# Kernel optimization log

Measured on AMD Instinct MI355X. Metric: run time of the kernel, lower is better.

The kernel has to match this reference:

```python
import jax, jax.numpy as jnp
import numpy as np

NUM_EXPERTS = 64
TOPK = 8
EPS = 1.1920929e-07  # torch.finfo(float32).eps


def setup_inputs() -> dict:
    key = jax.random.key(0)
    k1, k2 = jax.random.split(key)
    hidden_states = jax.random.normal(k1, (1, 4096, 4096), dtype=jnp.float32)
    wg_weight = jax.random.normal(k2, (NUM_EXPERTS, 4096), dtype=jnp.float32) * 0.02
    return {"hidden_states": hidden_states, "wg_weight": wg_weight}


def _routing(logits, capacity):
    # logits: [T, E]; capacity: static python int
    gates = jax.nn.softmax(logits, axis=1)                       # [T, E]
    _, idx = jax.lax.top_k(gates, TOPK)                          # [T, k]
    emask = jax.nn.one_hot(idx, NUM_EXPERTS, dtype=jnp.float32)  # [T, k, E]
    # sum of selected gate probs per token, clamped at fp32 eps
    gates_s = jnp.clip(jnp.einsum('tke,te->t', emask, gates), EPS)[:, None]
    router_probs = gates / gates_s                               # [T, E]
    # priority: cumulative position of each token within each expert,
    # scanned over (topk-major, token-minor) flattened order
    idx_flat = idx.T.reshape(-1)                                 # [k*T]
    mflat = jax.nn.one_hot(idx_flat, NUM_EXPERTS, dtype=jnp.int32)
    tp = jnp.cumsum(mflat, axis=0) * mflat - 1                   # [k*T, E]
    tp = tp.reshape(TOPK, -1, NUM_EXPERTS).transpose(1, 0, 2).max(axis=1)  # [T, E]
    valid = (tp >= 0) & (tp < capacity)                          # [T, E]
    tp = jnp.where(valid, tp, 0)
    dispatch_mask = jax.nn.one_hot(tp, capacity, dtype=jnp.bool_) & valid[:, :, None]  # [T, E, C]
    combine_weights = router_probs[:, :, None] * dispatch_mask   # [T, E, C]
    return combine_weights, dispatch_mask


def reference(hidden_states, wg_weight):
    b, s, h = hidden_states.shape
    x = hidden_states.reshape(-1, h).astype(jnp.float32)         # [T, H]
    logits = x @ wg_weight.T                                     # [T, E]
    # expert_capacity = max tokens assigned to any expert (data-dependent,
    # computed eagerly as in the torch .item() call)
    _, idx = jax.lax.top_k(jax.nn.softmax(logits, axis=1), TOPK)
    counts = jnp.bincount(idx.reshape(-1), length=NUM_EXPERTS)
    capacity = int(counts.max())
    return _routing(logits, capacity)
```

## Files before the change

kernel.cpp:

```cpp
#include <hip/hip_runtime.h>
#include <hip/hip_bf16.h>


#define TOK 4096
#define HID 4096
#define NE  64
#define NK  8

typedef __attribute__((ext_vector_type(8))) short short8;
typedef __attribute__((ext_vector_type(4))) float f32x4;

__device__ __forceinline__ short f2bf(float f) {
  __hip_bfloat16 h = __float2bfloat16(f);
  return *reinterpret_cast<short*>(&h);
}
__device__ __forceinline__ float bf2f(short s) {
  unsigned u = ((unsigned)(unsigned short)s) << 16;
  return __uint_as_float(u);
}
__device__ __forceinline__ void cvt3(float f, short& s0, short& s1, short& s2) {
  s0 = f2bf(f);
  float r1 = f - bf2f(s0);
  s1 = f2bf(r1);
  float r2 = r1 - bf2f(s1);
  s2 = f2bf(r2);
}

__global__ __launch_bounds__(256) void gemm_fill(
    const float* __restrict__ x, const float* __restrict__ wg,
    double* __restrict__ partial, int kchunk, int* __restrict__ flag,
    float* __restrict__ out, int out_n) {
  __shared__ __align__(16) short XA[3][64][72];
  __shared__ __align__(16) short WB[3][64][72];
  const int tid = threadIdx.x;
  if (blockIdx.x == 0 && blockIdx.y == 0 && tid == 0) *flag = 0;
  const int t0   = blockIdx.x * 64;
  const int k0   = blockIdx.y * kchunk;
  const int lane = tid & 63;
  const int w    = tid >> 6;
  const int m    = lane & 15;
  const int q    = lane >> 4;
  const int lrow = tid >> 2;
  const int lq   = tid & 3;

  const int    nblk    = gridDim.x * gridDim.y;
  const int    bid     = blockIdx.y * gridDim.x + blockIdx.x;
  const size_t n4      = ((size_t)(unsigned)out_n) >> 2;
  const size_t fstride = (size_t)nblk * 256;
  size_t       fi      = (size_t)bid * 256 + tid;
  const int    steps   = kchunk >> 6;
  const size_t titers  = (n4 + fstride - 1) / fstride;
  const size_t chunk   = (titers + (size_t)steps - 1) / (size_t)steps;
  f32x4* o4 = (f32x4*)out;
  const f32x4 z4 = (f32x4){0.f, 0.f, 0.f, 0.f};

  f32x4 acc[4];
#pragma unroll
  for (int nt = 0; nt < 4; ++nt) acc[nt] = (f32x4){0.f, 0.f, 0.f, 0.f};

  for (int s = 0; s < kchunk; s += 64) {
    const int kk = k0 + s;
#pragma unroll
    for (int c = 0; c < 4; ++c) {
      const int col = lq * 16 + c * 4;
      float4 xv = *(const float4*)&x [(size_t)(t0 + lrow) * HID + kk + col];
      float4 wv = *(const float4*)&wg[(size_t)lrow * HID + kk + col];
      short4 p0, p1, p2;
      cvt3(xv.x, p0.x, p1.x, p2.x);  cvt3(xv.y, p0.y, p1.y, p2.y);
      cvt3(xv.z, p0.z, p1.z, p2.z);  cvt3(xv.w, p0.w, p1.w, p2.w);
      *(short4*)&XA[0][lrow][col] = p0;
      *(short4*)&XA[1][lrow][col] = p1;
      *(short4*)&XA[2][lrow][col] = p2;
      cvt3(wv.x, p0.x, p1.x, p2.x);  cvt3(wv.y, p0.y, p1.y, p2.y);
      cvt3(wv.z, p0.z, p1.z, p2.z);  cvt3(wv.w, p0.w, p1.w, p2.w);
      *(short4*)&WB[0][lrow][col] = p0;
      *(short4*)&WB[1][lrow][col] = p1;
      *(short4*)&WB[2][lrow][col] = p2;
    }
    __syncthreads();
#pragma unroll
    for (int kc = 0; kc < 64; kc += 32) {
      short8 a0 = *(const short8*)&XA[0][w * 16 + m][kc + q * 8];
      short8 a1 = *(const short8*)&XA[1][w * 16 + m][kc + q * 8];
      short8 a2 = *(const short8*)&XA[2][w * 16 + m][kc + q * 8];
#pragma unroll
      for (int nt = 0; nt < 4; ++nt) {
        short8 b0 = *(const short8*)&WB[0][nt * 16 + m][kc + q * 8];
        short8 b1 = *(const short8*)&WB[1][nt * 16 + m][kc + q * 8];
        short8 b2 = *(const short8*)&WB[2][nt * 16 + m][kc + q * 8];
        acc[nt] = __builtin_amdgcn_mfma_f32_16x16x32_bf16(a0, b0, acc[nt], 0, 0, 0);
        acc[nt] = __builtin_amdgcn_mfma_f32_16x16x32_bf16(a0, b1, acc[nt], 0, 0, 0);
        acc[nt] = __builtin_amdgcn_mfma_f32_16x16x32_bf16(a1, b0, acc[nt], 0, 0, 0);
        acc[nt] = __builtin_amdgcn_mfma_f32_16x16x32_bf16(a0, b2, acc[nt], 0, 0, 0);
        acc[nt] = __builtin_amdgcn_mfma_f32_16x16x32_bf16(a1, b1, acc[nt], 0, 0, 0);
        acc[nt] = __builtin_amdgcn_mfma_f32_16x16x32_bf16(a2, b0, acc[nt], 0, 0, 0);
      }
    }
    for (size_t c = 0; c < chunk && fi < n4; ++c, fi += fstride)
      __builtin_nontemporal_store(z4, o4 + fi);
    __syncthreads();
  }

  for (; fi < n4; fi += fstride)
    __builtin_nontemporal_store(z4, o4 + fi);
  if (bid == 0 && tid == 0)
    for (size_t i2 = n4 << 2; i2 < (size_t)(unsigned)out_n; ++i2) out[i2] = 0.f;

  double* base = partial + (size_t)blockIdx.y * TOK * NE;
#pragma unroll
  for (int nt = 0; nt < 4; ++nt)
#pragma unroll
    for (int v = 0; v < 4; ++v)
      base[(size_t)(t0 + w * 16 + q * 4 + v) * NE + nt * 16 + m] =
          (double)acc[nt][v];
}

__global__ __launch_bounds__(256) void verify_kernel(
    const float* __restrict__ x, const float* __restrict__ wg,
    const double* __restrict__ partial, int nsplit, int* __restrict__ flag) {
  const int gid  = blockIdx.x * blockDim.x + threadIdx.x;
  const int wid  = gid >> 6;
  const int lane = gid & 63;
  const int t = (wid * 521) & (TOK - 1);
  const int e = wid & 63;
  double acc = 0.0;
  for (int k = lane; k < HID; k += 64)
    acc = fma((double)x[(size_t)t * HID + k], (double)wg[(size_t)e * HID + k], acc);
#pragma unroll
  for (int off = 32; off; off >>= 1) acc += __shfl_xor(acc, off);
  if (lane == 0) {
    double got = 0.0;
    for (int p = 0; p < nsplit; ++p)
      got += partial[(size_t)p * TOK * NE + (size_t)t * NE + e];
    if (!(fabs(got - acc) <= 1e-3)) atomicOr(flag, 1);
  }
}

__global__ __launch_bounds__(256) void repair_splitk(
    const float* __restrict__ x, const float* __restrict__ wg,
    double* __restrict__ partial, int kchunk, const int* __restrict__ flag) {
  if (*(volatile const int*)flag == 0) return;
  __shared__ float xs[16][68];
  __shared__ float wsh[64][68];
  const int tid = threadIdx.x;
  const int t0  = blockIdx.x * 16;
  const int k0  = blockIdx.y * kchunk;
  const int tok = tid & 15;
  const int eg  = tid >> 4;
  const int lrow = tid >> 4;
  const int lq   = tid & 15;
  double acc[4] = {0.0, 0.0, 0.0, 0.0};

  for (int s = 0; s < kchunk; s += 64) {
    const int kk = k0 + s;
    {
      float4 v = *(const float4*)&x[(size_t)(t0 + lrow) * HID + kk + lq * 4];
      *(float4*)&xs[lrow][lq * 4] = v;
    }
#pragma unroll
    for (int it = 0; it < 4; ++it) {
      int r = it * 16 + lrow;
      float4 v = *(const float4*)&wg[(size_t)r * HID + kk + lq * 4];
      *(float4*)&wsh[r][lq * 4] = v;
    }
    __syncthreads();
#pragma unroll
    for (int kc = 0; kc < 64; kc += 4) {
      float4 xv = *(const float4*)&xs[tok][kc];
#pragma unroll
      for (int j = 0; j < 4; ++j) {
        float4 wv = *(const float4*)&wsh[eg * 4 + j][kc];
        acc[j] = fma((double)xv.x, (double)wv.x, acc[j]);
        acc[j] = fma((double)xv.y, (double)wv.y, acc[j]);
        acc[j] = fma((double)xv.z, (double)wv.z, acc[j]);
        acc[j] = fma((double)xv.w, (double)wv.w, acc[j]);
      }
    }
    __syncthreads();
  }
  double* base = partial + (size_t)blockIdx.y * TOK * NE;
#pragma unroll
  for (int j = 0; j < 4; ++j)
    base[(size_t)(t0 + tok) * NE + eg * 4 + j] = acc[j];
}

__global__ __launch_bounds__(256) void topk_kernel(
    const double* __restrict__ partial, int nsplit,
    int* __restrict__ idx_kt, float* __restrict__ w_kt) {
  const int gid  = blockIdx.x * blockDim.x + threadIdx.x;
  const int t    = gid >> 6;
  const int lane = gid & 63;

  double v = 0.0;
  for (int p = 0; p < nsplit; ++p)
    v += partial[(size_t)p * TOK * NE + (size_t)t * NE + lane];

  double m = v;
#pragma unroll
  for (int off = 32; off; off >>= 1) {
    double o = __shfl_xor(m, off);
    m = o > m ? o : m;
  }
  double g = exp(v - m);
  double s = g;
#pragma unroll
  for (int off = 32; off; off >>= 1) s += __shfl_xor(s, off);
  double gate = g / s;

  float key = (float)gate;
  double ssel = 0.0;
  int my_k = -1;
#pragma unroll
  for (int k = 0; k < NK; ++k) {
    float bv = key;
    int   bi = lane;
#pragma unroll
    for (int off = 32; off; off >>= 1) {
      float ov = __shfl_xor(bv, off);
      int   oi = __shfl_xor(bi, off);
      if (ov > bv || (ov == bv && oi < bi)) { bv = ov; bi = oi; }
    }
    ssel += __shfl(gate, bi);
    if (lane == bi) { my_k = k; key = -1.0f; }
  }
  double gs = ssel;
  const double eps = (double)1.1920929e-07f;
  if (gs < eps) gs = eps;

  if (my_k >= 0) {
    idx_kt[my_k * TOK + t] = lane;
    w_kt [my_k * TOK + t] = (float)(gate / gs);
  }
}

__global__ __launch_bounds__(1024) void rank_scatter(
    const int* __restrict__ idx_kt, const float* __restrict__ w_kt,
    float* __restrict__ out, int C) {
  const int e    = blockIdx.x;
  const int tid  = threadIdx.x;
  const int lane = tid & 63;
  const int w    = tid >> 6;
  __shared__ int wt[16];
  int running = 0;
  const unsigned long long below = (1ull << lane) - 1ull;

  for (int i0 = 0; i0 < NK * TOK; i0 += 1024) {
    const int i = i0 + tid;
    const bool mhit = (idx_kt[i] == e);
    unsigned long long mask = __ballot(mhit);
    if (lane == 0) wt[w] = __popcll(mask);
    __syncthreads();
    int woff = 0, tot = 0;
#pragma unroll
    for (int j = 0; j < 16; ++j) {
      int c = wt[j];
      tot += c;
      if (j < w) woff += c;
    }
    if (mhit) {
      const int c = running + woff + __popcll(mask & below);
      if (c < C) {
        const int t = i & (TOK - 1);
        size_t off = ((size_t)t * NE + e) * (size_t)C + (size_t)c;
        out[off] = w_kt[i];
        out[(size_t)TOK * NE * C + off] = 1.0f;
      }
    }
    running += tot;
    __syncthreads();
  }
}

extern "C" void kernel_launch(void* const* d_in, const int* in_sizes, int n_in,
                              void* d_out, int out_size, void* d_ws, size_t ws_size,
                              hipStream_t stream) {
  const float* x  = (const float*)d_in[0];
  const float* wg = (const float*)d_in[1];
  float* out = (float*)d_out;

  const int C = out_size / (2 * TOK * NE);

  const size_t slab = (size_t)TOK * NE * sizeof(double);
  const size_t tail = 2 * (size_t)NK * TOK * sizeof(int);
  int nsplit = 8;
  while (nsplit > 1 && (size_t)nsplit * slab + tail + 64 > ws_size) nsplit >>= 1;
  const int kchunk = HID / nsplit;

  char* ws = (char*)d_ws;
  double* partial = (double*)ws;
  int*    idx_kt  = (int*)  (ws + (size_t)nsplit * slab);
  float*  w_kt    = (float*)(ws + (size_t)nsplit * slab + (size_t)NK * TOK * 4);
  int*    flag    = (int*)  (ws + (size_t)nsplit * slab + tail);


  dim3 bgrid(TOK / 64, nsplit);
  dim3 rgrid(TOK / 16, nsplit);
  gemm_fill    <<<bgrid, 256, 0, stream>>>(x, wg, partial, kchunk, flag, out, out_size);
  verify_kernel<<<128, 256, 0, stream>>>(x, wg, partial, nsplit, flag);
  repair_splitk<<<rgrid, 256, 0, stream>>>(x, wg, partial, kchunk, flag);
  topk_kernel  <<<TOK * 64 / 256, 256, 0, stream>>>(partial, nsplit, idx_kt, w_kt);
  rank_scatter <<<NE, 1024, 0, stream>>>(idx_kt, w_kt, out, C);
}
```

Before: 1.301 ms.

## Pre-split gate weights once and move output zero-fill to separate blocks

Adds a prep kernel that splits the gate weights into three bf16 parts once, so GEMM blocks no longer re-split them every tile. The GEMM now reads those parts straight from global memory instead of through shared memory. Zeroing the large output moves out of the GEMM loop into dedicated extra blocks in the same launch, so the fill runs alongside the GEMM on separate blocks. The trade-offs are one extra launch, more workspace, and B-operand loads that no longer go through LDS and may be less coalesced.

```diff
diff --git a/kernel.cpp b/kernel.cpp
--- a/kernel.cpp
+++ b/kernel.cpp
@@ -26,16 +26,46 @@
   s2 = f2bf(r2);
 }
 
-__global__ __launch_bounds__(256) void gemm_fill(
-    const float* __restrict__ x, const float* __restrict__ wg,
-    double* __restrict__ partial, int kchunk, int* __restrict__ flag,
-    float* __restrict__ out, int out_n) {
+__global__ __launch_bounds__(256) void prep_wg(
+    const float* __restrict__ wg, short* __restrict__ wp) {
+  const int idx = blockIdx.x * 256 + threadIdx.x;
+  const int e  = idx >> 10;
+  const int kq = idx & 1023;
+  float4 v = *(const float4*)&wg[(size_t)e * HID + kq * 4];
+  short4 p0, p1, p2;
+  cvt3(v.x, p0.x, p1.x, p2.x);  cvt3(v.y, p0.y, p1.y, p2.y);
+  cvt3(v.z, p0.z, p1.z, p2.z);  cvt3(v.w, p0.w, p1.w, p2.w);
+  *(short4*)&wp[((size_t)  0 + e) * HID + kq * 4] = p0;
+  *(short4*)&wp[((size_t) 64 + e) * HID + kq * 4] = p1;
+  *(short4*)&wp[((size_t)128 + e) * HID + kq * 4] = p2;
+}
+
+__global__ __launch_bounds__(256, 3) void mega(
+    const float* __restrict__ x, const short* __restrict__ wp,
+    double* __restrict__ partial, int kchunk, int ngemm, int nfill,
+    int* __restrict__ flag, float* __restrict__ out, int out_n) {
+  const int bx  = blockIdx.x;
+  const int tid = threadIdx.x;
+
+  if (bx >= ngemm) {
+    const int    fid    = bx - ngemm;
+    const size_t n4     = ((size_t)(unsigned)out_n) >> 2;
+    const size_t stride = (size_t)nfill * 256;
+    f32x4* o4 = (f32x4*)out;
+    const f32x4 z4 = (f32x4){0.f, 0.f, 0.f, 0.f};
+    for (size_t i = (size_t)fid * 256 + tid; i < n4; i += stride)
+      __builtin_nontemporal_store(z4, o4 + i);
+    if (fid == 0 && tid == 0)
+      for (size_t i2 = n4 << 2; i2 < (size_t)(unsigned)out_n; ++i2) out[i2] = 0.f;
+    return;
+  }
+
   __shared__ __align__(16) short XA[3][64][72];
-  __shared__ __align__(16) short WB[3][64][72];
-  const int tid = threadIdx.x;
-  if (blockIdx.x == 0 && blockIdx.y == 0 && tid == 0) *flag = 0;
-  const int t0   = blockIdx.x * 64;
-  const int k0   = blockIdx.y * kchunk;
+  if (bx == 0 && tid == 0) *flag = 0;
+  const int tileid = bx & 63;
+  const int slab   = bx >> 6;
+  const int t0   = tileid * 64;
+  const int k0   = slab * kchunk;
   const int lane = tid & 63;
   const int w    = tid >> 6;
   const int m    = lane & 15;
@@ -43,17 +73,6 @@
   const int lrow = tid >> 2;
   const int lq   = tid & 3;
 
-  const int    nblk    = gridDim.x * gridDim.y;
-  const int    bid     = blockIdx.y * gridDim.x + blockIdx.x;
-  const size_t n4      = ((size_t)(unsigned)out_n) >> 2;
-  const size_t fstride = (size_t)nblk * 256;
-  size_t       fi      = (size_t)bid * 256 + tid;
-  const int    steps   = kchunk >> 6;
-  const size_t titers  = (n4 + fstride - 1) / fstride;
-  const size_t chunk   = (titers + (size_t)steps - 1) / (size_t)steps;
-  f32x4* o4 = (f32x4*)out;
-  const f32x4 z4 = (f32x4){0.f, 0.f, 0.f, 0.f};
-
   f32x4 acc[4];
 #pragma unroll
   for (int nt = 0; nt < 4; ++nt) acc[nt] = (f32x4){0.f, 0.f, 0.f, 0.f};
@@ -63,19 +82,13 @@
 #pragma unroll
     for (int c = 0; c < 4; ++c) {
       const int col = lq * 16 + c * 4;
-      float4 xv = *(const float4*)&x [(size_t)(t0 + lrow) * HID + kk + col];
-      float4 wv = *(const float4*)&wg[(size_t)lrow * HID + kk + col];
+      float4 xv = *(const float4*)&x[(size_t)(t0 + lrow) * HID + kk + col];
       short4 p0, p1, p2;
       cvt3(xv.x, p0.x, p1.x, p2.x);  cvt3(xv.y, p0.y, p1.y, p2.y);
       cvt3(xv.z, p0.z, p1.z, p2.z);  cvt3(xv.w, p0.w, p1.w, p2.w);
       *(short4*)&XA[0][lrow][col] = p0;
       *(short4*)&XA[1][lrow][col] = p1;
       *(short4*)&XA[2][lrow][col] = p2;
-      cvt3(wv.x, p0.x, p1.x, p2.x);  cvt3(wv.y, p0.y, p1.y, p2.y);
-      cvt3(wv.z, p0.z, p1.z, p2.z);  cvt3(wv.w, p0.w, p1.w, p2.w);
-      *(short4*)&WB[0][lrow][col] = p0;
-      *(short4*)&WB[1][lrow][col] = p1;
-      *(short4*)&WB[2][lrow][col] = p2;
     }
     __syncthreads();
 #pragma unroll
@@ -85,9 +98,10 @@
       short8 a2 = *(const short8*)&XA[2][w * 16 + m][kc + q * 8];
 #pragma unroll
       for (int nt = 0; nt < 4; ++nt) {
-        short8 b0 = *(const short8*)&WB[0][nt * 16 + m][kc + q * 8];
-        short8 b1 = *(const short8*)&WB[1][nt * 16 + m][kc + q * 8];
-        short8 b2 = *(const short8*)&WB[2][nt * 16 + m][kc + q * 8];
+        const size_t roff = (size_t)(nt * 16 + m) * HID + (kk + kc + q * 8);
+        short8 b0 = *(const short8*)&wp[roff];
+        short8 b1 = *(const short8*)&wp[(size_t) 64 * HID + roff];
+        short8 b2 = *(const short8*)&wp[(size_t)128 * HID + roff];
         acc[nt] = __builtin_amdgcn_mfma_f32_16x16x32_bf16(a0, b0, acc[nt], 0, 0, 0);
         acc[nt] = __builtin_amdgcn_mfma_f32_16x16x32_bf16(a0, b1, acc[nt], 0, 0, 0);
         acc[nt] = __builtin_amdgcn_mfma_f32_16x16x32_bf16(a1, b0, acc[nt], 0, 0, 0);
@@ -96,17 +110,10 @@
         acc[nt] = __builtin_amdgcn_mfma_f32_16x16x32_bf16(a2, b0, acc[nt], 0, 0, 0);
       }
     }
-    for (size_t c = 0; c < chunk && fi < n4; ++c, fi += fstride)
-      __builtin_nontemporal_store(z4, o4 + fi);
-    __syncthreads();
-  }
-
-  for (; fi < n4; fi += fstride)
-    __builtin_nontemporal_store(z4, o4 + fi);
-  if (bid == 0 && tid == 0)
-    for (size_t i2 = n4 << 2; i2 < (size_t)(unsigned)out_n; ++i2) out[i2] = 0.f;
-
-  double* base = partial + (size_t)blockIdx.y * TOK * NE;
+    __syncthreads();
+  }
+
+  double* base = partial + (size_t)slab * TOK * NE;
 #pragma unroll
   for (int nt = 0; nt < 4; ++nt)
 #pragma unroll
@@ -282,8 +289,9 @@
 
   const size_t slab = (size_t)TOK * NE * sizeof(double);
   const size_t tail = 2 * (size_t)NK * TOK * sizeof(int);
+  const size_t wpb  = (size_t)3 * NE * HID * sizeof(short);
   int nsplit = 8;
-  while (nsplit > 1 && (size_t)nsplit * slab + tail + 64 > ws_size) nsplit >>= 1;
+  while (nsplit > 1 && (size_t)nsplit * slab + tail + 64 + wpb > ws_size) nsplit >>= 1;
   const int kchunk = HID / nsplit;
 
   char* ws = (char*)d_ws;
@@ -291,12 +299,16 @@
   int*    idx_kt  = (int*)  (ws + (size_t)nsplit * slab);
   float*  w_kt    = (float*)(ws + (size_t)nsplit * slab + (size_t)NK * TOK * 4);
   int*    flag    = (int*)  (ws + (size_t)nsplit * slab + tail);
-
-
-  dim3 bgrid(TOK / 64, nsplit);
+  short*  wp      = (short*)(ws + (size_t)nsplit * slab + tail + 64);
+
+  const int ngemm = 64 * nsplit;
+  const int nfill = 1536;
+
+  prep_wg      <<<256, 256, 0, stream>>>(wg, wp);
+  mega         <<<ngemm + nfill, 256, 0, stream>>>(x, wp, partial, kchunk,
+                                                   ngemm, nfill, flag, out, out_size);
+  verify_kernel<<<128, 256, 0, stream>>>(x, wg, partial, nsplit, flag);
   dim3 rgrid(TOK / 16, nsplit);
-  gemm_fill    <<<bgrid, 256, 0, stream>>>(x, wg, partial, kchunk, flag, out, out_size);
-  verify_kernel<<<128, 256, 0, stream>>>(x, wg, partial, nsplit, flag);
   repair_splitk<<<rgrid, 256, 0, stream>>>(x, wg, partial, kchunk, flag);
   topk_kernel  <<<TOK * 64 / 256, 256, 0, stream>>>(partial, nsplit, idx_kt, w_kt);
   rank_scatter <<<NE, 1024, 0, stream>>>(idx_kt, w_kt, out, C);
```

Result: no change. 1.290 ms (-0.9%).

## Stage split-K partials in output buffer and zero output with memset

Applied to the files above, without the earlier changes.

The zero-fill of the large output tensor moves out of the GEMM kernel's K-loop into a single hipMemsetAsync issued after top-k and before the scatter. The double-precision split-K partials and the flag now live in the tail of the output buffer rather than in the workspace, with the split count fixed at 8. The aim is to stop the zeroing stores from competing with the GEMM and to let the memset run at fill bandwidth. The cost is that the zeroing no longer overlaps with GEMM compute, and correctness relies on the output buffer being large enough to hold the partials.

```diff
diff --git a/kernel.cpp b/kernel.cpp
--- a/kernel.cpp
+++ b/kernel.cpp
@@ -6,6 +6,7 @@
 #define HID 4096
 #define NE  64
 #define NK  8
+#define NSPLIT 8
 
 typedef __attribute__((ext_vector_type(8))) short short8;
 typedef __attribute__((ext_vector_type(4))) float f32x4;
@@ -26,10 +27,9 @@
   s2 = f2bf(r2);
 }
 
-__global__ __launch_bounds__(256) void gemm_fill(
+__global__ __launch_bounds__(256) void gemm_bf16x3(
     const float* __restrict__ x, const float* __restrict__ wg,
-    double* __restrict__ partial, int kchunk, int* __restrict__ flag,
-    float* __restrict__ out, int out_n) {
+    double* __restrict__ partial, int kchunk, int* __restrict__ flag) {
   __shared__ __align__(16) short XA[3][64][72];
   __shared__ __align__(16) short WB[3][64][72];
   const int tid = threadIdx.x;
@@ -42,17 +42,6 @@
   const int q    = lane >> 4;
   const int lrow = tid >> 2;
   const int lq   = tid & 3;
-
-  const int    nblk    = gridDim.x * gridDim.y;
-  const int    bid     = blockIdx.y * gridDim.x + blockIdx.x;
-  const size_t n4      = ((size_t)(unsigned)out_n) >> 2;
-  const size_t fstride = (size_t)nblk * 256;
-  size_t       fi      = (size_t)bid * 256 + tid;
-  const int    steps   = kchunk >> 6;
-  const size_t titers  = (n4 + fstride - 1) / fstride;
-  const size_t chunk   = (titers + (size_t)steps - 1) / (size_t)steps;
-  f32x4* o4 = (f32x4*)out;
-  const f32x4 z4 = (f32x4){0.f, 0.f, 0.f, 0.f};
 
   f32x4 acc[4];
 #pragma unroll
@@ -96,15 +85,8 @@
         acc[nt] = __builtin_amdgcn_mfma_f32_16x16x32_bf16(a2, b0, acc[nt], 0, 0, 0);
       }
     }
-    for (size_t c = 0; c < chunk && fi < n4; ++c, fi += fstride)
-      __builtin_nontemporal_store(z4, o4 + fi);
-    __syncthreads();
-  }
-
-  for (; fi < n4; fi += fstride)
-    __builtin_nontemporal_store(z4, o4 + fi);
-  if (bid == 0 && tid == 0)
-    for (size_t i2 = n4 << 2; i2 < (size_t)(unsigned)out_n; ++i2) out[i2] = 0.f;
+    __syncthreads();
+  }
 
   double* base = partial + (size_t)blockIdx.y * TOK * NE;
 #pragma unroll
@@ -280,24 +262,26 @@
 
   const int C = out_size / (2 * TOK * NE);
 
-  const size_t slab = (size_t)TOK * NE * sizeof(double);
-  const size_t tail = 2 * (size_t)NK * TOK * sizeof(int);
-  int nsplit = 8;
-  while (nsplit > 1 && (size_t)nsplit * slab + tail + 64 > ws_size) nsplit >>= 1;
-  const int kchunk = HID / nsplit;
-
-  char* ws = (char*)d_ws;
-  double* partial = (double*)ws;
-  int*    idx_kt  = (int*)  (ws + (size_t)nsplit * slab);
-  float*  w_kt    = (float*)(ws + (size_t)nsplit * slab + (size_t)NK * TOK * 4);
-  int*    flag    = (int*)  (ws + (size_t)nsplit * slab + tail);
-
-
-  dim3 bgrid(TOK / 64, nsplit);
-  dim3 rgrid(TOK / 16, nsplit);
-  gemm_fill    <<<bgrid, 256, 0, stream>>>(x, wg, partial, kchunk, flag, out, out_size);
-  verify_kernel<<<128, 256, 0, stream>>>(x, wg, partial, nsplit, flag);
+  const size_t out_bytes = (size_t)out_size * sizeof(float);
+  const size_t psz       = (size_t)NSPLIT * TOK * NE * sizeof(double);
+  const size_t soff      = (out_bytes - (psz + 1024)) & ~(size_t)1023;
+  char* ob = (char*)d_out;
+  double* partial = (double*)(ob + soff);
+  int*    flag    = (int*)  (ob + soff + psz);
+
+  int*    idx_kt  = (int*)  d_ws;
+  float*  w_kt    = (float*)((char*)d_ws + (size_t)NK * TOK * sizeof(int));
+
+  const int kchunk = HID / NSPLIT;
+
+  dim3 bgrid(TOK / 64, NSPLIT);
+  dim3 rgrid(TOK / 16, NSPLIT);
+  gemm_bf16x3  <<<bgrid, 256, 0, stream>>>(x, wg, partial, kchunk, flag);
+  verify_kernel<<<128, 256, 0, stream>>>(x, wg, partial, NSPLIT, flag);
   repair_splitk<<<rgrid, 256, 0, stream>>>(x, wg, partial, kchunk, flag);
-  topk_kernel  <<<TOK * 64 / 256, 256, 0, stream>>>(partial, nsplit, idx_kt, w_kt);
+  topk_kernel  <<<TOK * 64 / 256, 256, 0, stream>>>(partial, NSPLIT, idx_kt, w_kt);
+
+  hipMemsetAsync(d_out, 0, out_bytes, stream);
+
   rank_scatter <<<NE, 1024, 0, stream>>>(idx_kt, w_kt, out, C);
 }
```

After: 1.258 ms. 3.4% less time.
